# Kernel tuning notes

Hardware: AMD Instinct MI355X
Metric: run time of the kernel (lower is better)

Reference implementation:

```python
import jax, jax.numpy as jnp
import numpy as np

# Module config (init_kwargs) and input dims
N, H, W, C = 8, 256, 256, 32
OH, OW = 512, 512  # size = (OH, OW); square so the original's H/W-swap quirks are benign


def setup_inputs() -> dict:
    key = jax.random.key(0)
    img = jax.random.normal(key, (N, H, W, C), dtype=jnp.float32)
    return {"img": img}


def reference(img):
    # Replicates BilinearInterpolate.build + call for square in/out sizes.
    _, H_, W_, _ = img.shape
    y_scale = H_ / OH
    x_scale = W_ / OW

    # Source sampling coordinates (half-pixel-center convention, clamped at 0)
    gy = jnp.maximum((jnp.arange(OH, dtype=jnp.float32) + 0.5) * y_scale - 0.5, 0.0)[:, None]  # (OH,1)
    gx = jnp.maximum((jnp.arange(OW, dtype=jnp.float32) + 0.5) * x_scale - 0.5, 0.0)[None, :]  # (1,OW)

    y0 = jnp.floor(gy).astype(jnp.int32)  # (OH,1)
    x0 = jnp.floor(gx).astype(jnp.int32)  # (1,OW)
    # Original guards the y-increment with W-1 and the x-increment with H-1 (swapped);
    # with H == W this is identical to the correct bounds.
    y1 = y0 + (y0 < W_ - 1).astype(jnp.int32)
    x1 = x0 + (x0 < H_ - 1).astype(jnp.int32)

    # Four-corner gather; advanced indexing broadcasts (OH,1)x(1,OW) -> (OH,OW),
    # result per corner is (N, OH, OW, C).
    v00 = img[:, y0, x0, :]
    v01 = img[:, y0, x1, :]  # +x
    v10 = img[:, y1, x0, :]  # +y
    v11 = img[:, y1, x1, :]

    # Fractional weights: h0 = y frac, w0 = x frac (matches l[...,0]/l[...,1])
    h0 = (gy - y0.astype(jnp.float32))[None, :, :, None]  # (1,OH,1,1)
    w0 = (gx - x0.astype(jnp.float32))[None, :, :, None]  # (1,1,OW,1)
    h1 = 1.0 - h0
    w1 = 1.0 - w0

    return h1 * (w1 * v00 + w0 * v01) + h0 * (w1 * v10 + w0 * v11)
```

## Files before the change

### kernel.cpp

```cpp
#include <hip/hip_runtime.h>


#define IH 256
#define IW 256
#define OHW 512
#define C4 8
#define JPER 16

typedef float f4 __attribute__((ext_vector_type(4)));

__global__ __launch_bounds__(256, 8) void bilinear2x_kernel(
    const float* __restrict__ img, float* __restrict__ out) {
    unsigned bx  = blockIdx.x;
    unsigned oxc = bx & 15u;
    unsigned jc  = (bx >> 4) & 15u;
    unsigned n   = bx >> 8;

    unsigned c4  = threadIdx.x & (C4 - 1);
    unsigned oxl = threadIdx.x >> 3;
    unsigned ox  = oxc * 32u + oxl;
    int j0 = (int)(jc * JPER);

    float gx = fmaxf(0.5f * (float)ox - 0.25f, 0.0f);
    int x0 = (int)gx;
    float w0 = gx - (float)x0;
    int x1 = x0 + (x0 < IW - 1);
    float w1 = 1.0f - w0;

    const f4* base = (const f4*)img + (size_t)n * (IH * IW * C4);
    size_t o0 = (size_t)x0 * C4 + c4;
    size_t o1 = (size_t)x1 * C4 + c4;

    int rA = j0 - 1; if (rA < 0) rA = 0;
    const f4* pA = base + (size_t)rA * (IW * C4);
    const f4* pB = base + (size_t)j0 * (IW * C4);
    f4 a0 = pA[o0], a1 = pA[o1];
    f4 b0 = pB[o0], b1 = pB[o1];
    f4 xa = w1 * a0 + w0 * a1;
    f4 xb = w1 * b0 + w0 * b1;

    f4* ob = (f4*)out;
    size_t oe = (((size_t)n * OHW + 2 * (size_t)j0) * OHW + ox) * C4 + c4;
    const size_t rowstep = (size_t)OHW * C4;

#pragma unroll 4
    for (int t = 0; t < JPER; ++t) {
        int j = j0 + t;
        int rC = j + 1; if (rC > IH - 1) rC = IH - 1;
        const f4* pC = base + (size_t)rC * (IW * C4);
        f4 cc0 = pC[o0], cc1 = pC[o1];
        f4 xc = w1 * cc0 + w0 * cc1;

        f4 re = 0.25f * xa + 0.75f * xb;
        f4 ro = 0.75f * xb + 0.25f * xc;
        ob[oe] = re;
        ob[oe + rowstep] = ro;
        oe += 2 * rowstep;

        xa = xb; xb = xc;
    }
}

extern "C" void kernel_launch(void* const* d_in, const int* in_sizes, int n_in,
                              void* d_out, int out_size, void* d_ws, size_t ws_size,
                              hipStream_t stream) {
    const float* img = (const float*)d_in[0];
    float* out = (float*)d_out;
    dim3 grid(2048);
    dim3 block(256);
    bilinear2x_kernel<<<grid, block, 0, stream>>>(img, out);
}
```

Before: 320.1 us.

## Restructure blocks to process full output row pairs instead of vertical strips

Each block now covers two input rows across the full output width, looping over 16 x-chunks. Previously each thread walked 16 rows down a vertical strip and reused the horizontally interpolated rows. The new layout reloads three input rows per output row pair, so vertical reuse is lost. In exchange it gets contiguous row-wise writes, a grid of 1024 blocks, and no minimum-occupancy hint in launch bounds.

```diff
diff --git a/kernel.cpp b/kernel.cpp
--- a/kernel.cpp
+++ b/kernel.cpp
@@ -5,59 +5,57 @@
 #define IW 256
 #define OHW 512
 #define C4 8
-#define JPER 16
 
 typedef float f4 __attribute__((ext_vector_type(4)));
 
-__global__ __launch_bounds__(256, 8) void bilinear2x_kernel(
+__global__ __launch_bounds__(256) void bilinear2x_kernel(
     const float* __restrict__ img, float* __restrict__ out) {
-    unsigned bx  = blockIdx.x;
-    unsigned oxc = bx & 15u;
-    unsigned jc  = (bx >> 4) & 15u;
-    unsigned n   = bx >> 8;
+    unsigned bx = blockIdx.x;
+    unsigned jc = bx & 127u;
+    unsigned n  = bx >> 7;
 
     unsigned c4  = threadIdx.x & (C4 - 1);
     unsigned oxl = threadIdx.x >> 3;
-    unsigned ox  = oxc * 32u + oxl;
-    int j0 = (int)(jc * JPER);
-
-    float gx = fmaxf(0.5f * (float)ox - 0.25f, 0.0f);
-    int x0 = (int)gx;
-    float w0 = gx - (float)x0;
-    int x1 = x0 + (x0 < IW - 1);
-    float w1 = 1.0f - w0;
 
     const f4* base = (const f4*)img + (size_t)n * (IH * IW * C4);
-    size_t o0 = (size_t)x0 * C4 + c4;
-    size_t o1 = (size_t)x1 * C4 + c4;
-
-    int rA = j0 - 1; if (rA < 0) rA = 0;
-    const f4* pA = base + (size_t)rA * (IW * C4);
-    const f4* pB = base + (size_t)j0 * (IW * C4);
-    f4 a0 = pA[o0], a1 = pA[o1];
-    f4 b0 = pB[o0], b1 = pB[o1];
-    f4 xa = w1 * a0 + w0 * a1;
-    f4 xb = w1 * b0 + w0 * b1;
-
     f4* ob = (f4*)out;
-    size_t oe = (((size_t)n * OHW + 2 * (size_t)j0) * OHW + ox) * C4 + c4;
     const size_t rowstep = (size_t)OHW * C4;
 
+    for (int tj = 0; tj < 2; ++tj) {
+        int j = (int)(jc * 2u) + tj;
+        int rA = j - 1; if (rA < 0) rA = 0;
+        int rC = j + 1; if (rC > IH - 1) rC = IH - 1;
+        const f4* pA = base + (size_t)rA * (IW * C4);
+        const f4* pB = base + (size_t)j  * (IW * C4);
+        const f4* pC = base + (size_t)rC * (IW * C4);
+        size_t oeRow = ((size_t)n * OHW + 2 * (size_t)j) * rowstep + c4;
+
 #pragma unroll 4
-    for (int t = 0; t < JPER; ++t) {
-        int j = j0 + t;
-        int rC = j + 1; if (rC > IH - 1) rC = IH - 1;
-        const f4* pC = base + (size_t)rC * (IW * C4);
-        f4 cc0 = pC[o0], cc1 = pC[o1];
-        f4 xc = w1 * cc0 + w0 * cc1;
+        for (int oxc = 0; oxc < 16; ++oxc) {
+            unsigned ox = (unsigned)oxc * 32u + oxl;
+            float gx = fmaxf(0.5f * (float)ox - 0.25f, 0.0f);
+            int x0 = (int)gx;
+            float w0 = gx - (float)x0;
+            int x1 = x0 + (x0 < IW - 1);
+            float w1 = 1.0f - w0;
+            size_t o0 = (size_t)x0 * C4 + c4;
+            size_t o1 = (size_t)x1 * C4 + c4;
 
-        f4 re = 0.25f * xa + 0.75f * xb;
-        f4 ro = 0.75f * xb + 0.25f * xc;
-        ob[oe] = re;
-        ob[oe + rowstep] = ro;
-        oe += 2 * rowstep;
+            f4 a0 = pA[o0], a1 = pA[o1];
+            f4 b0 = pB[o0], b1 = pB[o1];
+            f4 c0 = pC[o0], c1 = pC[o1];
 
-        xa = xb; xb = xc;
+            f4 ra = w1 * a0 + w0 * a1;
+            f4 rb = w1 * b0 + w0 * b1;
+            f4 rc = w1 * c0 + w0 * c1;
+
+            f4 re = 0.25f * ra + 0.75f * rb;
+            f4 ro = 0.75f * rb + 0.25f * rc;
+
+            size_t oe = oeRow + (size_t)ox * C4;
+            ob[oe] = re;
+            ob[oe + rowstep] = ro;
+        }
     }
 }
 
@@ -66,7 +64,7 @@
                               hipStream_t stream) {
     const float* img = (const float*)d_in[0];
     float* out = (float*)d_out;
-    dim3 grid(2048);
+    dim3 grid(1024);
     dim3 block(256);
     bilinear2x_kernel<<<grid, block, 0, stream>>>(img, out);
 }
```

New measurement: 331.3 us. +3.5%, slower.
